# Optimization experiments

Hardware: AMD Instinct MI355X
Metric: run time of the kernel (lower is better)

Reference implementation:

```python
import jax, jax.numpy as jnp
import numpy as np

N, E = 50000, 800000
IN_DIM, HID, OUT_DIM, HEADS = 256, 128, 128, 2
EPS_BN = 1e-5


def _glorot(key, shape):
    fan_in, fan_out = shape[0], shape[-1]
    lim = float(np.sqrt(6.0 / (fan_in + fan_out)))
    return jax.random.uniform(key, shape, jnp.float32, -lim, lim)


def setup_inputs() -> dict:
    key = jax.random.key(0)
    ks = jax.random.split(key, 12)
    x = jax.random.normal(ks[0], (N, IN_DIM), jnp.float32)
    edge_index = jax.random.randint(ks[1], (2, E), 0, N, jnp.int64)
    return {
        "x": x,
        "edge_index": edge_index,
        # layer 1 (heads=2, concat)
        "W1": _glorot(ks[2], (IN_DIM, HEADS * HID)),
        "att_src1": _glorot(ks[3], (HEADS, HID)),
        "att_dst1": _glorot(ks[4], (HEADS, HID)),
        "b1": jnp.zeros((HEADS * HID,), jnp.float32),
        "g1": jnp.ones((HEADS * HID,), jnp.float32),
        "be1": jnp.zeros((HEADS * HID,), jnp.float32),
        # layer 2 (heads=1, no concat)
        "W2": _glorot(ks[5], (HEADS * HID, OUT_DIM)),
        "att_src2": _glorot(ks[6], (1, OUT_DIM)),
        "att_dst2": _glorot(ks[7], (1, OUT_DIM)),
        "b2": jnp.zeros((OUT_DIM,), jnp.float32),
        "g2": jnp.ones((OUT_DIM,), jnp.float32),
        "be2": jnp.zeros((OUT_DIM,), jnp.float32),
    }


def gat_conv(x, src, dst, W, att_src, att_dst, bias, heads, out_ch, concat):
    """PyG GATConv forward (dropout=identity at eval). Messages flow src->dst,
    softmax over incoming edges of dst, sum-aggregate."""
    h = (x @ W).reshape(-1, heads, out_ch)             # [N, H, C]
    a_s = jnp.einsum('nhc,hc->nh', h, att_src)          # [N, H]
    a_d = jnp.einsum('nhc,hc->nh', h, att_dst)
    e = jax.nn.leaky_relu(a_s[src] + a_d[dst], 0.2)     # [E, H]
    m = jax.ops.segment_max(e, dst, num_segments=N)     # [N, H]
    m = jnp.where(jnp.isfinite(m), m, 0.0)
    w = jnp.exp(e - m[dst])                             # [E, H]
    denom = jax.ops.segment_sum(w, dst, num_segments=N) # [N, H]
    alpha = w / (denom[dst] + 1e-16)                    # [E, H]
    msg = h[src] * alpha[:, :, None]                    # [E, H, C]
    out = jax.ops.segment_sum(msg, dst, num_segments=N) # [N, H, C]
    if concat:
        out = out.reshape(-1, heads * out_ch)
    else:
        out = out.mean(axis=1)
    return out + bias


def batchnorm_relu(x, gamma, beta):
    mu = x.mean(axis=0)
    var = x.var(axis=0)  # biased, as used for normalization in torch BN
    xn = (x - mu) * jax.lax.rsqrt(var + EPS_BN)
    return jax.nn.relu(xn * gamma + beta)


def reference(x, edge_index, W1, att_src1, att_dst1, b1, g1, be1,
              W2, att_src2, att_dst2, b2, g2, be2):
    src, dst = edge_index[0], edge_index[1]
    h = gat_conv(x, src, dst, W1, att_src1, att_dst1, b1, HEADS, HID, True)
    h = batchnorm_relu(h, g1, be1)
    h = gat_conv(h, src, dst, W2, att_src2, att_dst2, b2, 1, OUT_DIM, False)
    h = batchnorm_relu(h, g2, be2)
    return h
```

## Files before the change

kernel.cpp:

```cpp
#include <hip/hip_runtime.h>
#include <math.h>

#define IN_DIM 256
#define EPS_BN 1e-5f
#define NS 16

typedef __attribute__((ext_vector_type(8))) short short8v;
typedef __attribute__((ext_vector_type(4))) float f32x4;

__device__ __forceinline__ float lrelu(float v) { return v > 0.f ? v : 0.2f * v; }

__device__ __forceinline__ unsigned short f2bf(float f) {
    unsigned int u = __float_as_uint(f);
    u += 0x7fffu + ((u >> 16) & 1u);
    return (unsigned short)(u >> 16);
}
__device__ __forceinline__ float bf2f(unsigned short s) {
    return __uint_as_float((unsigned int)s << 16);
}

__device__ __forceinline__ void gld16(const void* g, void* l) {
    __builtin_amdgcn_global_load_lds((const __attribute__((address_space(1))) void*)g,
                                     (__attribute__((address_space(3))) void*)l, 16, 0, 0);
}

__device__ __forceinline__ int edge_at(const void* ei, int is64, long long i) {
    if (is64) return (int)((const long long*)ei)[i];
    return ((const int*)ei)[i];
}

__global__ __launch_bounds__(256) void prep_kernel(const float* __restrict__ x,
                                                   unsigned short* __restrict__ xb, long long n8,
                                                   const float* __restrict__ W1,
                                                   unsigned short* __restrict__ Wt1,
                                                   const float* __restrict__ W2,
                                                   unsigned short* __restrict__ Wt2,
                                                   const unsigned int* __restrict__ eiw,
                                                   int* __restrict__ flag, long long nwords) {
    __shared__ int nz;
    long long nbx = (n8 + 255) / 256;
    long long b = blockIdx.x;
    if (b < nbx) {
        long long i = b * 256 + threadIdx.x;
        if (i < n8) {
            const float4* p = (const float4*)(x + i * 8);
            float4 v0 = p[0], v1 = p[1];
            ushort4 o0, o1;
            o0.x = f2bf(v0.x); o0.y = f2bf(v0.y); o0.z = f2bf(v0.z); o0.w = f2bf(v0.w);
            o1.x = f2bf(v1.x); o1.y = f2bf(v1.y); o1.z = f2bf(v1.z); o1.w = f2bf(v1.w);
            *(ushort4*)(xb + i * 8) = o0;
            *(ushort4*)(xb + i * 8 + 4) = o1;
        }
        return;
    }
    b -= nbx;
    if (b < 256) {
        int idx = (int)b * 256 + threadIdx.x;
        int c = idx >> 8, k = idx & 255;
        Wt1[idx] = f2bf(W1[(long long)k * 256 + c]);
        return;
    }
    b -= 256;
    if (b < 128) {
        int idx = (int)b * 256 + threadIdx.x;
        int c = idx >> 8, k = idx & 255;
        Wt2[idx] = f2bf(W2[(long long)k * 128 + c]);
        return;
    }
    if (threadIdx.x == 0) nz = 0;
    __syncthreads();
    int cnt = 0;
    for (int i = 0; i < 4; i++) {
        long long idx = 2LL * (threadIdx.x + i * 256) + 1;
        if (idx < nwords && eiw[idx] != 0u) cnt++;
    }
    if (cnt) atomicAdd(&nz, 1);
    __syncthreads();
    if (threadIdx.x == 0) flag[0] = (nz == 0) ? 1 : 0;
}

__global__ void count_deg_kernel(const void* __restrict__ ei, const int* __restrict__ flag,
                                 int* __restrict__ deg, int E_) {
    int is64 = flag[0];
    int i = blockIdx.x * 256 + threadIdx.x;
    if (i < E_) {
        int d = edge_at(ei, is64, (long long)E_ + i);
        atomicAdd(&deg[d], 1);
    }
}

__global__ __launch_bounds__(256) void scan_partial_kernel(const int* __restrict__ deg,
                                                           int* __restrict__ bsum, int n) {
    __shared__ int sh[256];
    int t = threadIdx.x;
    int i = blockIdx.x * 256 + t;
    sh[t] = (i < n) ? deg[i] : 0;
    __syncthreads();
    for (int off = 128; off >= 1; off >>= 1) {
        if (t < off) sh[t] += sh[t + off];
        __syncthreads();
    }
    if (t == 0) bsum[blockIdx.x] = sh[0];
}

__global__ __launch_bounds__(256) void scan_write_kernel(const int* __restrict__ deg,
                                                         const int* __restrict__ bsum,
                                                         int* __restrict__ rowptr,
                                                         int* __restrict__ ctr, int n, int nb) {
    __shared__ int sh[256];
    __shared__ int base_sh;
    int t = threadIdx.x;
    int b = blockIdx.x;
    sh[t] = (t < b) ? bsum[t] : 0;
    __syncthreads();
    for (int off = 128; off >= 1; off >>= 1) {
        if (t < off) sh[t] += sh[t + off];
        __syncthreads();
    }
    if (t == 0) base_sh = sh[0];
    __syncthreads();
    int i = b * 256 + t;
    int d = (i < n) ? deg[i] : 0;
    sh[t] = d;
    __syncthreads();
    for (int off = 1; off < 256; off <<= 1) {
        int u = (t >= off) ? sh[t - off] : 0;
        __syncthreads();
        sh[t] += u;
        __syncthreads();
    }
    if (i < n) {
        int v = base_sh + sh[t] - d;
        rowptr[i] = v;
        ctr[i] = v;
    }
    if (b == nb - 1 && t == 255) rowptr[n] = base_sh + sh[255];
}

__global__ void scatter_kernel(const void* __restrict__ ei, const int* __restrict__ flag,
                               int* __restrict__ ctr, int* __restrict__ srcs, int E_) {
    int is64 = flag[0];
    int i = blockIdx.x * 256 + threadIdx.x;
    if (i < E_) {
        int s = edge_at(ei, is64, i);
        int d = edge_at(ei, is64, (long long)E_ + i);
        int pos = atomicAdd(&ctr[d], 1);
        srcs[pos] = s;
    }
}

template <int NCOL, int NH, bool FUSEBN>
__global__ __launch_bounds__(256) void gemm_mfma_kernel(const unsigned short* __restrict__ Ab,
                                                        const unsigned short* __restrict__ Wt,
                                                        unsigned short* __restrict__ C,
                                                        const float* __restrict__ att_s,
                                                        const float* __restrict__ att_d,
                                                        float* __restrict__ a_s,
                                                        float* __restrict__ a_d, int M,
                                                        const float* __restrict__ bnsh,
                                                        const float* __restrict__ gamma,
                                                        const float* __restrict__ beta) {
    __shared__ unsigned short B_lds[64 * 256];
    __shared__ unsigned short A_lds[128 * 64];
    __shared__ float scs[FUSEBN ? 256 : 1];
    __shared__ float shs[FUSEBN ? 256 : 1];
    const int t = threadIdx.x;
    const int w = t >> 6, l = t & 63;
    const int row0 = blockIdx.x * 128;
    const int col0 = blockIdx.y * 64;

    {
        const char* wb = (const char*)Wt + (size_t)col0 * 512;
#pragma unroll
        for (int it = 0; it < 8; ++it) {
            int q = w * 8 + it;
            int i = q * 64 + l;
            int r = i >> 5;
            int cs = (i & 31) ^ (r & 7);
            gld16(wb + (size_t)r * 512 + cs * 16, (char*)B_lds + q * 1024);
        }
    }

    short8v nxt[4];
    const char* ab = (const char*)Ab + (size_t)row0 * 512;

    if (FUSEBN) {
        {
            int c = t;
            float s = 0.f, q = 0.f;
#pragma unroll
            for (int sh = 0; sh < NS; sh++) { s += bnsh[sh * 512 + c]; q += bnsh[sh * 512 + 256 + c]; }
            float invN = 1.f / (float)M;
            float mu = s * invN;
            float var = q * invN - mu * mu;
            float sc = rsqrtf(var + EPS_BN) * gamma[c];
            scs[c] = sc;
            shs[c] = beta[c] - mu * sc;
        }
#pragma unroll
        for (int it = 0; it < 4; ++it) {
            int i = it * 256 + t;
            int r = i >> 3, g = i & 7;
            int gr = row0 + r;
            nxt[it] = (gr < M) ? *(const short8v*)(Ab + (size_t)gr * 256 + g * 8)
                               : (short8v)(short)0;
        }
        __syncthreads();
#pragma unroll
        for (int it = 0; it < 4; ++it) {
            int i = it * 256 + t;
            int r = i >> 3, g = i & 7;
            int kb = g * 8;
            float4 s0 = *(const float4*)&scs[kb], s1 = *(const float4*)&scs[kb + 4];
            float4 h0 = *(const float4*)&shs[kb], h1 = *(const float4*)&shs[kb + 4];
            short8v v = nxt[it];
            short8v ov;
            ov[0] = (short)f2bf(fmaxf(bf2f((unsigned short)v[0]) * s0.x + h0.x, 0.f));
            ov[1] = (short)f2bf(fmaxf(bf2f((unsigned short)v[1]) * s0.y + h0.y, 0.f));
            ov[2] = (short)f2bf(fmaxf(bf2f((unsigned short)v[2]) * s0.z + h0.z, 0.f));
            ov[3] = (short)f2bf(fmaxf(bf2f((unsigned short)v[3]) * s0.w + h0.w, 0.f));
            ov[4] = (short)f2bf(fmaxf(bf2f((unsigned short)v[4]) * s1.x + h1.x, 0.f));
            ov[5] = (short)f2bf(fmaxf(bf2f((unsigned short)v[5]) * s1.y + h1.y, 0.f));
            ov[6] = (short)f2bf(fmaxf(bf2f((unsigned short)v[6]) * s1.z + h1.z, 0.f));
            ov[7] = (short)f2bf(fmaxf(bf2f((unsigned short)v[7]) * s1.w + h1.w, 0.f));
            *(short8v*)((char*)A_lds + r * 128 + ((g ^ (r & 7)) << 4)) = ov;
        }
    } else {
#pragma unroll
        for (int it = 0; it < 4; ++it) {
            int q = w * 4 + it;
            int i = q * 64 + l;
            int r = i >> 3;
            int cs = (i & 7) ^ (r & 7);
            gld16(ab + (size_t)r * 512 + cs * 16, (char*)A_lds + q * 1024);
        }
    }
    __syncthreads();

    const int rl = l & 15, kg = l >> 4;
    f32x4 acc0[4], acc1[4];
#pragma unroll
    for (int i = 0; i < 4; ++i) { acc0[i] = (f32x4)(0.f); acc1[i] = (f32x4)(0.f); }

    const int ar0 = w * 32 + rl, ar1 = ar0 + 16;
    const int aswz = (ar0 & 7) << 4;

    for (int c = 0; c < 4; ++c) {
        if (FUSEBN && c < 3) {
#pragma unroll
            for (int it = 0; it < 4; ++it) {
                int i = it * 256 + t;
                int r = i >> 3, g = i & 7;
                int gr = row0 + r;
                nxt[it] = (gr < M) ? *(const short8v*)(Ab + (size_t)gr * 256 + (c + 1) * 64 + g * 8)
                                   : (short8v)(short)0;
            }
        }
#pragma unroll
        for (int s = 0; s < 2; ++s) {
            short8v a0 = *(const short8v*)((const char*)A_lds +
                          ((ar0 * 128 + s * 64 + kg * 16) ^ aswz));
            short8v a1 = *(const short8v*)((const char*)A_lds +
                          ((ar1 * 128 + s * 64 + kg * 16) ^ aswz));
#pragma unroll
            for (int ct = 0; ct < 4; ++ct) {
                int br = ct * 16 + rl;
                short8v bfr = *(const short8v*)((const char*)B_lds +
                               ((br * 512 + c * 128 + s * 64 + kg * 16) ^ ((br & 7) << 4)));
                acc0[ct] = __builtin_amdgcn_mfma_f32_16x16x32_bf16(a0, bfr, acc0[ct], 0, 0, 0);
                acc1[ct] = __builtin_amdgcn_mfma_f32_16x16x32_bf16(a1, bfr, acc1[ct], 0, 0, 0);
            }
        }
        __syncthreads();
        if (c < 3) {
            if (FUSEBN) {
#pragma unroll
                for (int it = 0; it < 4; ++it) {
                    int i = it * 256 + t;
                    int r = i >> 3, g = i & 7;
                    int kb = (c + 1) * 64 + g * 8;
                    float4 s0 = *(const float4*)&scs[kb], s1 = *(const float4*)&scs[kb + 4];
                    float4 h0 = *(const float4*)&shs[kb], h1 = *(const float4*)&shs[kb + 4];
                    short8v v = nxt[it];
                    short8v ov;
                    ov[0] = (short)f2bf(fmaxf(bf2f((unsigned short)v[0]) * s0.x + h0.x, 0.f));
                    ov[1] = (short)f2bf(fmaxf(bf2f((unsigned short)v[1]) * s0.y + h0.y, 0.f));
                    ov[2] = (short)f2bf(fmaxf(bf2f((unsigned short)v[2]) * s0.z + h0.z, 0.f));
                    ov[3] = (short)f2bf(fmaxf(bf2f((unsigned short)v[3]) * s0.w + h0.w, 0.f));
                    ov[4] = (short)f2bf(fmaxf(bf2f((unsigned short)v[4]) * s1.x + h1.x, 0.f));
                    ov[5] = (short)f2bf(fmaxf(bf2f((unsigned short)v[5]) * s1.y + h1.y, 0.f));
                    ov[6] = (short)f2bf(fmaxf(bf2f((unsigned short)v[6]) * s1.z + h1.z, 0.f));
                    ov[7] = (short)f2bf(fmaxf(bf2f((unsigned short)v[7]) * s1.w + h1.w, 0.f));
                    *(short8v*)((char*)A_lds + r * 128 + ((g ^ (r & 7)) << 4)) = ov;
                }
            } else {
#pragma unroll
                for (int it = 0; it < 4; ++it) {
                    int q = w * 4 + it;
                    int i = q * 64 + l;
                    int r = i >> 3;
                    int cs = (i & 7) ^ (r & 7);
                    gld16(ab + (size_t)r * 512 + (c + 1) * 128 + cs * 16, (char*)A_lds + q * 1024);
                }
            }
            __syncthreads();
        }
    }

#pragma unroll
    for (int ct = 0; ct < 4; ++ct) {
#pragma unroll
        for (int r = 0; r < 4; ++r) {
            int gr0 = row0 + w * 32 + kg * 4 + r;
            if (gr0 < M) C[(long long)gr0 * NCOL + col0 + ct * 16 + rl] = f2bf(acc0[ct][r]);
            int gr1 = gr0 + 16;
            if (gr1 < M) C[(long long)gr1 * NCOL + col0 + ct * 16 + rl] = f2bf(acc1[ct][r]);
        }
    }

    float asp0[4] = {}, adp0[4] = {}, asp1[4] = {}, adp1[4] = {};
#pragma unroll
    for (int ct = 0; ct < 4; ++ct) {
        int col = col0 + ct * 16 + rl;
        float vs = att_s[col], vd = att_d[col];
#pragma unroll
        for (int r = 0; r < 4; ++r) {
            asp0[r] += acc0[ct][r] * vs; adp0[r] += acc0[ct][r] * vd;
            asp1[r] += acc1[ct][r] * vs; adp1[r] += acc1[ct][r] * vd;
        }
    }
#pragma unroll
    for (int off = 1; off < 16; off <<= 1) {
#pragma unroll
        for (int r = 0; r < 4; ++r) {
            asp0[r] += __shfl_xor(asp0[r], off);
            adp0[r] += __shfl_xor(adp0[r], off);
            asp1[r] += __shfl_xor(asp1[r], off);
            adp1[r] += __shfl_xor(adp1[r], off);
        }
    }
    if (rl == 0) {
        int head = (NH == 2) ? (col0 >> 7) : 0;
#pragma unroll
        for (int r = 0; r < 4; ++r) {
            int gr0 = row0 + w * 32 + kg * 4 + r;
            if (gr0 < M) {
                atomicAdd(&a_s[gr0 * NH + head], asp0[r]);
                atomicAdd(&a_d[gr0 * NH + head], adp0[r]);
            }
            int gr1 = gr0 + 16;
            if (gr1 < M) {
                atomicAdd(&a_s[gr1 * NH + head], asp1[r]);
                atomicAdd(&a_d[gr1 * NH + head], adp1[r]);
            }
        }
    }
}

__global__ __launch_bounds__(256) void aggregate1_kernel(const unsigned short* __restrict__ h,
                                                         const int* __restrict__ rowptr,
                                                         const int* __restrict__ srcs,
                                                         const float* __restrict__ a_s,
                                                         const float* __restrict__ a_d,
                                                         const float* __restrict__ bias,
                                                         unsigned short* __restrict__ out,
                                                         float* __restrict__ bnsh, int Nn) {
    __shared__ float sw_lds[4][256];
    const int t = threadIdx.x;
    const int wid = t >> 6, lane = t & 63;
    const int hh = (lane >> 4) & 1;
    const int eb = lane >> 5;
    const int colb = (lane & 31) * 8;
    float* wbase = sw_lds[wid];
    float bnsum[8] = {}, bnsq[8] = {};
    const int stride = gridDim.x * 4;

    for (int n = blockIdx.x * 4 + wid; n < Nn; n += stride) {
        int beg = rowptr[n], end = rowptr[n + 1];
        float2 adv = *(const float2*)&a_d[(size_t)n * 2];
        float ad0 = adv.x, ad1 = adv.y;
        float acc[8] = {0.f, 0.f, 0.f, 0.f, 0.f, 0.f, 0.f, 0.f};
        float den = 0.f, m0 = -1e30f, m1 = -1e30f;

        for (int cb = beg; cb < end; cb += 64) {
            int cnt = end - cb; if (cnt > 64) cnt = 64;
            float e0 = -1e30f, e1 = -1e30f;
            int s_l = 0;
            if (lane < cnt) {
                s_l = srcs[cb + lane];
                float2 av = *(const float2*)&a_s[(size_t)s_l * 2];
                e0 = lrelu(av.x + ad0);
                e1 = lrelu(av.y + ad1);
            }
            float cm0 = e0, cm1 = e1;
            for (int off = 32; off >= 1; off >>= 1) {
                cm0 = fmaxf(cm0, __shfl_xor(cm0, off));
                cm1 = fmaxf(cm1, __shfl_xor(cm1, off));
            }
            if (cm0 > m0 || cm1 > m1) {
                float f0 = (cm0 > m0) ? __expf(m0 - cm0) : 1.f;
                float f1 = (cm1 > m1) ? __expf(m1 - cm1) : 1.f;
                m0 = fmaxf(m0, cm0); m1 = fmaxf(m1, cm1);
                float fo = hh ? f1 : f0;
#pragma unroll
                for (int j = 0; j < 8; j++) acc[j] *= fo;
                den *= fo;
            }
            if (lane < cnt) {
                *(float2*)&wbase[lane * 2] = make_float2(__int_as_float(s_l), __expf(e0 - m0));
                *(float2*)&wbase[128 + lane * 2] = make_float2(__int_as_float(s_l), __expf(e1 - m1));
            }
            int c = 0;
            for (; c + 8 <= cnt; c += 8) {
                float2 sw0 = *(const float2*)&wbase[hh * 128 + (c + eb) * 2];
                float2 sw1 = *(const float2*)&wbase[hh * 128 + (c + 2 + eb) * 2];
                float2 sw2 = *(const float2*)&wbase[hh * 128 + (c + 4 + eb) * 2];
                float2 sw3 = *(const float2*)&wbase[hh * 128 + (c + 6 + eb) * 2];
                short8v p0 = *(const short8v*)(h + ((size_t)__float_as_int(sw0.x) << 8) + colb);
                short8v p1 = *(const short8v*)(h + ((size_t)__float_as_int(sw1.x) << 8) + colb);
                short8v p2 = *(const short8v*)(h + ((size_t)__float_as_int(sw2.x) << 8) + colb);
                short8v p3 = *(const short8v*)(h + ((size_t)__float_as_int(sw3.x) << 8) + colb);
                den += sw0.y + sw1.y + sw2.y + sw3.y;
#pragma unroll
                for (int j = 0; j < 8; j++)
                    acc[j] += sw0.y * bf2f((unsigned short)p0[j]) + sw1.y * bf2f((unsigned short)p1[j])
                            + sw2.y * bf2f((unsigned short)p2[j]) + sw3.y * bf2f((unsigned short)p3[j]);
            }
            for (; c + 4 <= cnt; c += 4) {
                float2 sw0 = *(const float2*)&wbase[hh * 128 + (c + eb) * 2];
                float2 sw1 = *(const float2*)&wbase[hh * 128 + (c + 2 + eb) * 2];
                short8v p0 = *(const short8v*)(h + ((size_t)__float_as_int(sw0.x) << 8) + colb);
                short8v p1 = *(const short8v*)(h + ((size_t)__float_as_int(sw1.x) << 8) + colb);
                den += sw0.y + sw1.y;
#pragma unroll
                for (int j = 0; j < 8; j++)
                    acc[j] += sw0.y * bf2f((unsigned short)p0[j]) + sw1.y * bf2f((unsigned short)p1[j]);
            }
            for (; c < cnt; c += 2) {
                int e = c + eb;
                if (e < cnt) {
                    float2 sw0 = *(const float2*)&wbase[hh * 128 + e * 2];
                    short8v p0 = *(const short8v*)(h + ((size_t)__float_as_int(sw0.x) << 8) + colb);
                    den += sw0.y;
#pragma unroll
                    for (int j = 0; j < 8; j++) acc[j] += sw0.y * bf2f((unsigned short)p0[j]);
                }
            }
        }
        den += __shfl_xor(den, 32);
#pragma unroll
        for (int j = 0; j < 8; j++) acc[j] += __shfl_xor(acc[j], 32);
        if (lane < 32) {
            float inv = 1.f / (den + 1e-16f);
            float4 b0 = *(const float4*)&bias[colb];
            float4 b1 = *(const float4*)&bias[colb + 4];
            float of[8];
            of[0] = acc[0] * inv + b0.x; of[1] = acc[1] * inv + b0.y;
            of[2] = acc[2] * inv + b0.z; of[3] = acc[3] * inv + b0.w;
            of[4] = acc[4] * inv + b1.x; of[5] = acc[5] * inv + b1.y;
            of[6] = acc[6] * inv + b1.z; of[7] = acc[7] * inv + b1.w;
            short8v o;
#pragma unroll
            for (int j = 0; j < 8; j++) {
                o[j] = (short)f2bf(of[j]);
                bnsum[j] += of[j];
                bnsq[j] += of[j] * of[j];
            }
            *(short8v*)(out + ((size_t)n << 8) + colb) = o;
        }
    }

    __syncthreads();
    if (lane < 32) {
#pragma unroll
        for (int j = 0; j < 8; j++) wbase[colb + j] = bnsum[j];
    }
    __syncthreads();
    {
        int sh = (blockIdx.x & (NS - 1)) * 512;
        float s = sw_lds[0][t] + sw_lds[1][t] + sw_lds[2][t] + sw_lds[3][t];
        atomicAdd(&bnsh[sh + t], s);
    }
    __syncthreads();
    if (lane < 32) {
#pragma unroll
        for (int j = 0; j < 8; j++) wbase[colb + j] = bnsq[j];
    }
    __syncthreads();
    {
        int sh = (blockIdx.x & (NS - 1)) * 512;
        float q = sw_lds[0][t] + sw_lds[1][t] + sw_lds[2][t] + sw_lds[3][t];
        atomicAdd(&bnsh[sh + 256 + t], q);
    }
}

__global__ __launch_bounds__(256) void aggregate2_kernel(const unsigned short* __restrict__ h,
                                                         const int* __restrict__ rowptr,
                                                         const int* __restrict__ srcs,
                                                         const float* __restrict__ a_s,
                                                         const float* __restrict__ a_d,
                                                         const float* __restrict__ bias,
                                                         float* __restrict__ out,
                                                         float* __restrict__ bnsh, int Nn) {
    __shared__ float sw_lds[4][128];
    const int t = threadIdx.x;
    const int wid = t >> 6, lane = t & 63;
    const int eo = lane >> 4;
    const int colb = (lane & 15) * 8;
    float* wbase = sw_lds[wid];
    float bnsum[8] = {}, bnsq[8] = {};
    const int stride = gridDim.x * 4;

    for (int n = blockIdx.x * 4 + wid; n < Nn; n += stride) {
        int beg = rowptr[n], end = rowptr[n + 1];
        float ad = a_d[n];
        float acc[8] = {0.f, 0.f, 0.f, 0.f, 0.f, 0.f, 0.f, 0.f};
        float den = 0.f, m = -1e30f;

        for (int cb = beg; cb < end; cb += 64) {
            int cnt = end - cb; if (cnt > 64) cnt = 64;
            float e_ = -1e30f;
            int s_l = 0;
            if (lane < cnt) {
                s_l = srcs[cb + lane];
                e_ = lrelu(a_s[s_l] + ad);
            }
            float cm = e_;
            for (int off = 32; off >= 1; off >>= 1) cm = fmaxf(cm, __shfl_xor(cm, off));
            if (cm > m) {
                float f = __expf(m - cm);
                m = cm;
#pragma unroll
                for (int j = 0; j < 8; j++) acc[j] *= f;
                den *= f;
            }
            if (lane < cnt)
                *(float2*)&wbase[lane * 2] = make_float2(__int_as_float(s_l), __expf(e_ - m));
            int c = 0;
            for (; c + 16 <= cnt; c += 16) {
                float2 sw0 = *(const float2*)&wbase[(c + eo) * 2];
                float2 sw1 = *(const float2*)&wbase[(c + 4 + eo) * 2];
                float2 sw2 = *(const float2*)&wbase[(c + 8 + eo) * 2];
                float2 sw3 = *(const float2*)&wbase[(c + 12 + eo) * 2];
                short8v p0 = *(const short8v*)(h + ((size_t)__float_as_int(sw0.x) << 7) + colb);
                short8v p1 = *(const short8v*)(h + ((size_t)__float_as_int(sw1.x) << 7) + colb);
                short8v p2 = *(const short8v*)(h + ((size_t)__float_as_int(sw2.x) << 7) + colb);
                short8v p3 = *(const short8v*)(h + ((size_t)__float_as_int(sw3.x) << 7) + colb);
                den += sw0.y + sw1.y + sw2.y + sw3.y;
#pragma unroll
                for (int j = 0; j < 8; j++)
                    acc[j] += sw0.y * bf2f((unsigned short)p0[j]) + sw1.y * bf2f((unsigned short)p1[j])
                            + sw2.y * bf2f((unsigned short)p2[j]) + sw3.y * bf2f((unsigned short)p3[j]);
            }
            for (; c + 8 <= cnt; c += 8) {
                float2 sw0 = *(const float2*)&wbase[(c + eo) * 2];
                float2 sw1 = *(const float2*)&wbase[(c + 4 + eo) * 2];
                short8v p0 = *(const short8v*)(h + ((size_t)__float_as_int(sw0.x) << 7) + colb);
                short8v p1 = *(const short8v*)(h + ((size_t)__float_as_int(sw1.x) << 7) + colb);
                den += sw0.y + sw1.y;
#pragma unroll
                for (int j = 0; j < 8; j++)
                    acc[j] += sw0.y * bf2f((unsigned short)p0[j]) + sw1.y * bf2f((unsigned short)p1[j]);
            }
            for (; c < cnt; c += 4) {
                int e = c + eo;
                if (e < cnt) {
                    float2 sw0 = *(const float2*)&wbase[e * 2];
                    short8v p0 = *(const short8v*)(h + ((size_t)__float_as_int(sw0.x) << 7) + colb);
                    den += sw0.y;
#pragma unroll
                    for (int j = 0; j < 8; j++) acc[j] += sw0.y * bf2f((unsigned short)p0[j]);
                }
            }
        }
        den += __shfl_xor(den, 16);
        den += __shfl_xor(den, 32);
#pragma unroll
        for (int j = 0; j < 8; j++) {
            acc[j] += __shfl_xor(acc[j], 16);
            acc[j] += __shfl_xor(acc[j], 32);
        }
        if (lane < 16) {
            float inv = 1.f / (den + 1e-16f);
            float4 b0 = *(const float4*)&bias[colb];
            float4 b1 = *(const float4*)&bias[colb + 4];
            float of[8];
            of[0] = acc[0] * inv + b0.x; of[1] = acc[1] * inv + b0.y;
            of[2] = acc[2] * inv + b0.z; of[3] = acc[3] * inv + b0.w;
            of[4] = acc[4] * inv + b1.x; of[5] = acc[5] * inv + b1.y;
            of[6] = acc[6] * inv + b1.z; of[7] = acc[7] * inv + b1.w;
#pragma unroll
            for (int j = 0; j < 8; j++) {
                bnsum[j] += of[j];
                bnsq[j] += of[j] * of[j];
            }
            float* ob = out + (size_t)n * 128 + colb;
            *(float4*)ob = make_float4(of[0], of[1], of[2], of[3]);
            *(float4*)(ob + 4) = make_float4(of[4], of[5], of[6], of[7]);
        }
    }

    __syncthreads();
    if (lane < 16) {
#pragma unroll
        for (int j = 0; j < 8; j++) wbase[colb + j] = bnsum[j];
    }
    __syncthreads();
    if (t < 128) {
        int sh = (blockIdx.x & (NS - 1)) * 256;
        float s = sw_lds[0][t] + sw_lds[1][t] + sw_lds[2][t] + sw_lds[3][t];
        atomicAdd(&bnsh[sh + t], s);
    }
    __syncthreads();
    if (lane < 16) {
#pragma unroll
        for (int j = 0; j < 8; j++) wbase[colb + j] = bnsq[j];
    }
    __syncthreads();
    if (t < 128) {
        int sh = (blockIdx.x & (NS - 1)) * 256;
        float q = sw_lds[0][t] + sw_lds[1][t] + sw_lds[2][t] + sw_lds[3][t];
        atomicAdd(&bnsh[sh + 128 + t], q);
    }
}

__global__ __launch_bounds__(256) void bn_apply_final_kernel(float* __restrict__ x,
                                                             const float* __restrict__ bnsh,
                                                             const float* __restrict__ gamma,
                                                             const float* __restrict__ beta,
                                                             int Nn) {
    int t = threadIdx.x;
    int col = t & 127;
    float s = 0.f, q = 0.f;
#pragma unroll
    for (int sh = 0; sh < NS; sh++) { s += bnsh[sh * 256 + col]; q += bnsh[sh * 256 + 128 + col]; }
    float mu = s / (float)Nn;
    float var = q / (float)Nn - mu * mu;
    float sc = rsqrtf(var + EPS_BN) * gamma[col];
    float sh_ = beta[col] - mu * sc;
    int r0 = blockIdx.x * 2 + (t >> 7);
    int rs = gridDim.x * 2;
    for (int r = r0; r < Nn; r += rs) {
        size_t idx = (size_t)r * 128 + col;
        x[idx] = fmaxf(x[idx] * sc + sh_, 0.f);
    }
}

extern "C" void kernel_launch(void* const* d_in, const int* in_sizes, int n_in,
                              void* d_out, int out_size, void* d_ws, size_t ws_size,
                              hipStream_t stream) {
    const float* x        = (const float*)d_in[0];
    const void*  ei       = d_in[1];
    const float* W1       = (const float*)d_in[2];
    const float* att_src1 = (const float*)d_in[3];
    const float* att_dst1 = (const float*)d_in[4];
    const float* b1       = (const float*)d_in[5];
    const float* g1       = (const float*)d_in[6];
    const float* be1      = (const float*)d_in[7];
    const float* W2       = (const float*)d_in[8];
    const float* att_src2 = (const float*)d_in[9];
    const float* att_dst2 = (const float*)d_in[10];
    const float* b2       = (const float*)d_in[11];
    const float* g2       = (const float*)d_in[12];
    const float* be2      = (const float*)d_in[13];

    const int Nn = in_sizes[0] / IN_DIM;
    const int E_ = in_sizes[1] / 2;
    const int gb = (Nn + 127) / 128;
    const int Mpad = gb * 128 + 128;

    char* ws = (char*)d_ws;
    size_t o = 0;
    auto alloc = [&](size_t bytes) {
        size_t r = o;
        o += (bytes + 255) & ~(size_t)255;
        return r;
    };
    int* flag = (int*)(ws + alloc(4));
    size_t z0 = o;
    int*   deg   = (int*)(ws + alloc((size_t)Nn * 4));
    float* as1   = (float*)(ws + alloc((size_t)Nn * 2 * 4));
    float* ad1   = (float*)(ws + alloc((size_t)Nn * 2 * 4));
    float* as2   = (float*)(ws + alloc((size_t)Nn * 4));
    float* ad2   = (float*)(ws + alloc((size_t)Nn * 4));
    float* bn1sh = (float*)(ws + alloc((size_t)NS * 512 * 4));
    float* bn2sh = (float*)(ws + alloc((size_t)NS * 256 * 4));
    size_t z1 = o;
    int*   rowptr = (int*)(ws + alloc((size_t)(Nn + 1) * 4));
    int*   ctr    = (int*)(ws + alloc((size_t)Nn * 4));
    int*   srcs   = (int*)(ws + alloc((size_t)E_ * 4));
    int*   bsum   = (int*)(ws + alloc(256 * 4));
    unsigned short* Wt1  = (unsigned short*)(ws + alloc((size_t)256 * 256 * 2));
    unsigned short* Wt2  = (unsigned short*)(ws + alloc((size_t)128 * 256 * 2));
    unsigned short* xb   = (unsigned short*)(ws + alloc((size_t)Mpad * 256 * 2));
    unsigned short* x2b0 = (unsigned short*)(ws + alloc((size_t)Nn * 256 * 2));
    unsigned short* h1b  = (unsigned short*)(ws + alloc((size_t)Nn * 256 * 2));
    unsigned short* h2b  = (unsigned short*)(ws + alloc((size_t)Nn * 128 * 2));
    float* outf = (float*)d_out;

    hipMemsetAsync(ws + z0, 0, z1 - z0, stream);

    {
        long long n8 = (long long)Nn * 256 / 8;
        long long grid = (n8 + 255) / 256 + 256 + 128 + 1;
        prep_kernel<<<(int)grid, 256, 0, stream>>>(x, xb, n8, W1, Wt1, W2, Wt2,
                                                   (const unsigned int*)ei, flag,
                                                   (long long)2 * E_);
    }

    int eb = (E_ + 255) / 256;
    int nsb = (Nn + 255) / 256;
    count_deg_kernel<<<eb, 256, 0, stream>>>(ei, flag, deg, E_);
    scan_partial_kernel<<<nsb, 256, 0, stream>>>(deg, bsum, Nn);
    scan_write_kernel<<<nsb, 256, 0, stream>>>(deg, bsum, rowptr, ctr, Nn, nsb);
    scatter_kernel<<<eb, 256, 0, stream>>>(ei, flag, ctr, srcs, E_);

    const int agg_blocks = 2048;

    gemm_mfma_kernel<256, 2, false><<<dim3(gb, 4), 256, 0, stream>>>(
        xb, Wt1, h1b, att_src1, att_dst1, as1, ad1, Nn, nullptr, nullptr, nullptr);
    aggregate1_kernel<<<agg_blocks, 256, 0, stream>>>(h1b, rowptr, srcs, as1, ad1, b1, x2b0,
                                                      bn1sh, Nn);

    gemm_mfma_kernel<128, 1, true><<<dim3(gb, 2), 256, 0, stream>>>(
        x2b0, Wt2, h2b, att_src2, att_dst2, as2, ad2, Nn, bn1sh, g1, be1);
    aggregate2_kernel<<<agg_blocks, 256, 0, stream>>>(h2b, rowptr, srcs, as2, ad2, b2, outf,
                                                      bn2sh, Nn);
    bn_apply_final_kernel<<<512, 256, 0, stream>>>(outf, bn2sh, g2, be2, Nn);
}
```

Before: 295.6 us.

## Merge CSR build and final BN into cooperative grid-synced kernels

Replaces the memset, prep, degree count, two-pass scan and scatter launches with one cooperative kernel that separates the phases with grid.sync, and folds the final batchnorm apply into the layer-2 aggregation kernel after a grid-wide sync. It also rewrites the bf16 accumulation in both aggregation kernels to unpack packed 32-bit words with shifts and masks into float2 FMAs. The aim is to cut kernel launch gaps and unpacking overhead, at the cost of persistent grids sized from occupancy, which may lower parallelism in the edge-heavy phases, plus the cost of each grid barrier.

Measured after the change: 924.9 us. 213% more time.

```diff
diff --git a/kernel.cpp b/kernel.cpp
--- a/kernel.cpp
+++ b/kernel.cpp
@@ -1,5 +1,8 @@
 #include <hip/hip_runtime.h>
+#include <hip/hip_cooperative_groups.h>
 #include <math.h>
+
+namespace cg = cooperative_groups;
 
 #define IN_DIM 256
 #define EPS_BN 1e-5f
@@ -19,6 +22,11 @@
     return __uint_as_float((unsigned int)s << 16);
 }
 
+__device__ __forceinline__ void bfma(float2& a, unsigned int pw, float w) {
+    a.x = fmaf(__uint_as_float(pw << 16), w, a.x);
+    a.y = fmaf(__uint_as_float(pw & 0xffff0000u), w, a.y);
+}
+
 __device__ __forceinline__ void gld16(const void* g, void* l) {
     __builtin_amdgcn_global_load_lds((const __attribute__((address_space(1))) void*)g,
                                      (__attribute__((address_space(3))) void*)l, 16, 0, 0);
@@ -29,119 +37,109 @@
     return ((const int*)ei)[i];
 }
 
-__global__ __launch_bounds__(256) void prep_kernel(const float* __restrict__ x,
-                                                   unsigned short* __restrict__ xb, long long n8,
-                                                   const float* __restrict__ W1,
-                                                   unsigned short* __restrict__ Wt1,
-                                                   const float* __restrict__ W2,
-                                                   unsigned short* __restrict__ Wt2,
-                                                   const unsigned int* __restrict__ eiw,
-                                                   int* __restrict__ flag, long long nwords) {
+__global__ __launch_bounds__(256) void build_kernel(
+    const float* __restrict__ x, unsigned short* __restrict__ xb, long long n8,
+    const float* __restrict__ W1, unsigned short* __restrict__ Wt1,
+    const float* __restrict__ W2, unsigned short* __restrict__ Wt2,
+    const void* __restrict__ ei, int* __restrict__ flag,
+    float* __restrict__ zbase, long long zcnt4,
+    int* __restrict__ deg, int* __restrict__ bsum,
+    int* __restrict__ rowptr, int* __restrict__ ctr, int* __restrict__ srcs,
+    int Nn, int E_, int nsb) {
+    __shared__ int sh[256];
+    __shared__ int base_sh;
     __shared__ int nz;
-    long long nbx = (n8 + 255) / 256;
-    long long b = blockIdx.x;
-    if (b < nbx) {
-        long long i = b * 256 + threadIdx.x;
-        if (i < n8) {
-            const float4* p = (const float4*)(x + i * 8);
-            float4 v0 = p[0], v1 = p[1];
-            ushort4 o0, o1;
-            o0.x = f2bf(v0.x); o0.y = f2bf(v0.y); o0.z = f2bf(v0.z); o0.w = f2bf(v0.w);
-            o1.x = f2bf(v1.x); o1.y = f2bf(v1.y); o1.z = f2bf(v1.z); o1.w = f2bf(v1.w);
-            *(ushort4*)(xb + i * 8) = o0;
-            *(ushort4*)(xb + i * 8 + 4) = o1;
-        }
-        return;
-    }
-    b -= nbx;
-    if (b < 256) {
-        int idx = (int)b * 256 + threadIdx.x;
-        int c = idx >> 8, k = idx & 255;
-        Wt1[idx] = f2bf(W1[(long long)k * 256 + c]);
-        return;
-    }
-    b -= 256;
-    if (b < 128) {
-        int idx = (int)b * 256 + threadIdx.x;
-        int c = idx >> 8, k = idx & 255;
-        Wt2[idx] = f2bf(W2[(long long)k * 128 + c]);
-        return;
-    }
-    if (threadIdx.x == 0) nz = 0;
-    __syncthreads();
-    int cnt = 0;
-    for (int i = 0; i < 4; i++) {
-        long long idx = 2LL * (threadIdx.x + i * 256) + 1;
-        if (idx < nwords && eiw[idx] != 0u) cnt++;
-    }
-    if (cnt) atomicAdd(&nz, 1);
-    __syncthreads();
-    if (threadIdx.x == 0) flag[0] = (nz == 0) ? 1 : 0;
-}
-
-__global__ void count_deg_kernel(const void* __restrict__ ei, const int* __restrict__ flag,
-                                 int* __restrict__ deg, int E_) {
-    int is64 = flag[0];
-    int i = blockIdx.x * 256 + threadIdx.x;
-    if (i < E_) {
+    const int t = threadIdx.x;
+    const int nb = gridDim.x;
+    const long long tstride = (long long)nb * 256;
+    cg::grid_group grid = cg::this_grid();
+
+    for (long long i = (long long)blockIdx.x * 256 + t; i < zcnt4; i += tstride)
+        *(float4*)(zbase + i * 4) = make_float4(0.f, 0.f, 0.f, 0.f);
+    const long long nbx = (n8 + 255) / 256;
+    const long long totA = nbx + 256 + 128 + 1;
+    for (long long vb = blockIdx.x; vb < totA; vb += nb) {
+        if (vb < nbx) {
+            long long i = vb * 256 + t;
+            if (i < n8) {
+                const float4* p = (const float4*)(x + i * 8);
+                float4 v0 = p[0], v1 = p[1];
+                ushort4 o0, o1;
+                o0.x = f2bf(v0.x); o0.y = f2bf(v0.y); o0.z = f2bf(v0.z); o0.w = f2bf(v0.w);
+                o1.x = f2bf(v1.x); o1.y = f2bf(v1.y); o1.z = f2bf(v1.z); o1.w = f2bf(v1.w);
+                *(ushort4*)(xb + i * 8) = o0;
+                *(ushort4*)(xb + i * 8 + 4) = o1;
+            }
+        } else if (vb < nbx + 256) {
+            int idx = (int)(vb - nbx) * 256 + t;
+            int c = idx >> 8, k = idx & 255;
+            Wt1[idx] = f2bf(W1[(long long)k * 256 + c]);
+        } else if (vb < nbx + 384) {
+            int idx = (int)(vb - nbx - 256) * 256 + t;
+            int c = idx >> 8, k = idx & 255;
+            Wt2[idx] = f2bf(W2[(long long)k * 128 + c]);
+        } else {
+            if (t == 0) nz = 0;
+            __syncthreads();
+            const unsigned int* w = (const unsigned int*)ei;
+            int cnt = 0;
+            for (int i2 = 0; i2 < 4; i2++) {
+                long long idx = 2LL * (t + i2 * 256) + 1;
+                if (idx < 2LL * E_ && w[idx] != 0u) cnt++;
+            }
+            if (cnt) atomicAdd(&nz, 1);
+            __syncthreads();
+            if (t == 0) flag[0] = (nz == 0) ? 1 : 0;
+        }
+    }
+    grid.sync();
+    const int is64 = flag[0];
+    for (long long i = (long long)blockIdx.x * 256 + t; i < E_; i += tstride) {
         int d = edge_at(ei, is64, (long long)E_ + i);
         atomicAdd(&deg[d], 1);
     }
-}
-
-__global__ __launch_bounds__(256) void scan_partial_kernel(const int* __restrict__ deg,
-                                                           int* __restrict__ bsum, int n) {
-    __shared__ int sh[256];
-    int t = threadIdx.x;
-    int i = blockIdx.x * 256 + t;
-    sh[t] = (i < n) ? deg[i] : 0;
-    __syncthreads();
-    for (int off = 128; off >= 1; off >>= 1) {
-        if (t < off) sh[t] += sh[t + off];
+    grid.sync();
+    for (int vb = blockIdx.x; vb < nsb; vb += nb) {
         __syncthreads();
-    }
-    if (t == 0) bsum[blockIdx.x] = sh[0];
-}
-
-__global__ __launch_bounds__(256) void scan_write_kernel(const int* __restrict__ deg,
-                                                         const int* __restrict__ bsum,
-                                                         int* __restrict__ rowptr,
-                                                         int* __restrict__ ctr, int n, int nb) {
-    __shared__ int sh[256];
-    __shared__ int base_sh;
-    int t = threadIdx.x;
-    int b = blockIdx.x;
-    sh[t] = (t < b) ? bsum[t] : 0;
-    __syncthreads();
-    for (int off = 128; off >= 1; off >>= 1) {
-        if (t < off) sh[t] += sh[t + off];
+        int i = vb * 256 + t;
+        sh[t] = (i < Nn) ? deg[i] : 0;
         __syncthreads();
-    }
-    if (t == 0) base_sh = sh[0];
-    __syncthreads();
-    int i = b * 256 + t;
-    int d = (i < n) ? deg[i] : 0;
-    sh[t] = d;
-    __syncthreads();
-    for (int off = 1; off < 256; off <<= 1) {
-        int u = (t >= off) ? sh[t - off] : 0;
+        for (int off = 128; off >= 1; off >>= 1) {
+            if (t < off) sh[t] += sh[t + off];
+            __syncthreads();
+        }
+        if (t == 0) bsum[vb] = sh[0];
+    }
+    grid.sync();
+    for (int vb = blockIdx.x; vb < nsb; vb += nb) {
         __syncthreads();
-        sh[t] += u;
+        sh[t] = (t < vb) ? bsum[t] : 0;
         __syncthreads();
-    }
-    if (i < n) {
-        int v = base_sh + sh[t] - d;
-        rowptr[i] = v;
-        ctr[i] = v;
-    }
-    if (b == nb - 1 && t == 255) rowptr[n] = base_sh + sh[255];
-}
-
-__global__ void scatter_kernel(const void* __restrict__ ei, const int* __restrict__ flag,
-                               int* __restrict__ ctr, int* __restrict__ srcs, int E_) {
-    int is64 = flag[0];
-    int i = blockIdx.x * 256 + threadIdx.x;
-    if (i < E_) {
+        for (int off = 128; off >= 1; off >>= 1) {
+            if (t < off) sh[t] += sh[t + off];
+            __syncthreads();
+        }
+        if (t == 0) base_sh = sh[0];
+        __syncthreads();
+        int i = vb * 256 + t;
+        int d = (i < Nn) ? deg[i] : 0;
+        sh[t] = d;
+        __syncthreads();
+        for (int off = 1; off < 256; off <<= 1) {
+            int u = (t >= off) ? sh[t - off] : 0;
+            __syncthreads();
+            sh[t] += u;
+            __syncthreads();
+        }
+        if (i < Nn) {
+            int v = base_sh + sh[t] - d;
+            rowptr[i] = v;
+            ctr[i] = v;
+        }
+        if (vb == nsb - 1 && t == 255) rowptr[Nn] = base_sh + sh[255];
+    }
+    grid.sync();
+    for (long long i = (long long)blockIdx.x * 256 + t; i < E_; i += tstride) {
         int s = edge_at(ei, is64, i);
         int d = edge_at(ei, is64, (long long)E_ + i);
         int pos = atomicAdd(&ctr[d], 1);
@@ -372,14 +370,14 @@
     const int eb = lane >> 5;
     const int colb = (lane & 31) * 8;
     float* wbase = sw_lds[wid];
-    float bnsum[8] = {}, bnsq[8] = {};
+    float2 bnsum2[4] = {}, bnsq2[4] = {};
     const int stride = gridDim.x * 4;
 
     for (int n = blockIdx.x * 4 + wid; n < Nn; n += stride) {
         int beg = rowptr[n], end = rowptr[n + 1];
         float2 adv = *(const float2*)&a_d[(size_t)n * 2];
         float ad0 = adv.x, ad1 = adv.y;
-        float acc[8] = {0.f, 0.f, 0.f, 0.f, 0.f, 0.f, 0.f, 0.f};
+        float2 acc2[4] = {};
         float den = 0.f, m0 = -1e30f, m1 = -1e30f;
 
         for (int cb = beg; cb < end; cb += 64) {
@@ -403,7 +401,7 @@
                 m0 = fmaxf(m0, cm0); m1 = fmaxf(m1, cm1);
                 float fo = hh ? f1 : f0;
 #pragma unroll
-                for (int j = 0; j < 8; j++) acc[j] *= fo;
+                for (int j = 0; j < 4; j++) { acc2[j].x *= fo; acc2[j].y *= fo; }
                 den *= fo;
             }
             if (lane < cnt) {
@@ -416,55 +414,65 @@
                 float2 sw1 = *(const float2*)&wbase[hh * 128 + (c + 2 + eb) * 2];
                 float2 sw2 = *(const float2*)&wbase[hh * 128 + (c + 4 + eb) * 2];
                 float2 sw3 = *(const float2*)&wbase[hh * 128 + (c + 6 + eb) * 2];
-                short8v p0 = *(const short8v*)(h + ((size_t)__float_as_int(sw0.x) << 8) + colb);
-                short8v p1 = *(const short8v*)(h + ((size_t)__float_as_int(sw1.x) << 8) + colb);
-                short8v p2 = *(const short8v*)(h + ((size_t)__float_as_int(sw2.x) << 8) + colb);
-                short8v p3 = *(const short8v*)(h + ((size_t)__float_as_int(sw3.x) << 8) + colb);
+                uint4 p0 = *(const uint4*)(h + ((size_t)__float_as_int(sw0.x) << 8) + colb);
+                uint4 p1 = *(const uint4*)(h + ((size_t)__float_as_int(sw1.x) << 8) + colb);
+                uint4 p2 = *(const uint4*)(h + ((size_t)__float_as_int(sw2.x) << 8) + colb);
+                uint4 p3 = *(const uint4*)(h + ((size_t)__float_as_int(sw3.x) << 8) + colb);
                 den += sw0.y + sw1.y + sw2.y + sw3.y;
-#pragma unroll
-                for (int j = 0; j < 8; j++)
-                    acc[j] += sw0.y * bf2f((unsigned short)p0[j]) + sw1.y * bf2f((unsigned short)p1[j])
-                            + sw2.y * bf2f((unsigned short)p2[j]) + sw3.y * bf2f((unsigned short)p3[j]);
+                bfma(acc2[0], p0.x, sw0.y); bfma(acc2[1], p0.y, sw0.y);
+                bfma(acc2[2], p0.z, sw0.y); bfma(acc2[3], p0.w, sw0.y);
+                bfma(acc2[0], p1.x, sw1.y); bfma(acc2[1], p1.y, sw1.y);
+                bfma(acc2[2], p1.z, sw1.y); bfma(acc2[3], p1.w, sw1.y);
+                bfma(acc2[0], p2.x, sw2.y); bfma(acc2[1], p2.y, sw2.y);
+                bfma(acc2[2], p2.z, sw2.y); bfma(acc2[3], p2.w, sw2.y);
+                bfma(acc2[0], p3.x, sw3.y); bfma(acc2[1], p3.y, sw3.y);
+                bfma(acc2[2], p3.z, sw3.y); bfma(acc2[3], p3.w, sw3.y);
             }
             for (; c + 4 <= cnt; c += 4) {
                 float2 sw0 = *(const float2*)&wbase[hh * 128 + (c + eb) * 2];
                 float2 sw1 = *(const float2*)&wbase[hh * 128 + (c + 2 + eb) * 2];
-                short8v p0 = *(const short8v*)(h + ((size_t)__float_as_int(sw0.x) << 8) + colb);
-                short8v p1 = *(const short8v*)(h + ((size_t)__float_as_int(sw1.x) << 8) + colb);
+                uint4 p0 = *(const uint4*)(h + ((size_t)__float_as_int(sw0.x) << 8) + colb);
+                uint4 p1 = *(const uint4*)(h + ((size_t)__float_as_int(sw1.x) << 8) + colb);
                 den += sw0.y + sw1.y;
-#pragma unroll
-                for (int j = 0; j < 8; j++)
-                    acc[j] += sw0.y * bf2f((unsigned short)p0[j]) + sw1.y * bf2f((unsigned short)p1[j]);
+                bfma(acc2[0], p0.x, sw0.y); bfma(acc2[1], p0.y, sw0.y);
+                bfma(acc2[2], p0.z, sw0.y); bfma(acc2[3], p0.w, sw0.y);
+                bfma(acc2[0], p1.x, sw1.y); bfma(acc2[1], p1.y, sw1.y);
+                bfma(acc2[2], p1.z, sw1.y); bfma(acc2[3], p1.w, sw1.y);
             }
             for (; c < cnt; c += 2) {
                 int e = c + eb;
                 if (e < cnt) {
                     float2 sw0 = *(const float2*)&wbase[hh * 128 + e * 2];
-                    short8v p0 = *(const short8v*)(h + ((size_t)__float_as_int(sw0.x) << 8) + colb);
+                    uint4 p0 = *(const uint4*)(h + ((size_t)__float_as_int(sw0.x) << 8) + colb);
                     den += sw0.y;
-#pragma unroll
-                    for (int j = 0; j < 8; j++) acc[j] += sw0.y * bf2f((unsigned short)p0[j]);
+                    bfma(acc2[0], p0.x, sw0.y); bfma(acc2[1], p0.y, sw0.y);
+                    bfma(acc2[2], p0.z, sw0.y); bfma(acc2[3], p0.w, sw0.y);
                 }
             }
         }
         den += __shfl_xor(den, 32);
 #pragma unroll
-        for (int j = 0; j < 8; j++) acc[j] += __shfl_xor(acc[j], 32);
+        for (int j = 0; j < 4; j++) {
+            acc2[j].x += __shfl_xor(acc2[j].x, 32);
+            acc2[j].y += __shfl_xor(acc2[j].y, 32);
+        }
         if (lane < 32) {
             float inv = 1.f / (den + 1e-16f);
             float4 b0 = *(const float4*)&bias[colb];
             float4 b1 = *(const float4*)&bias[colb + 4];
             float of[8];
-            of[0] = acc[0] * inv + b0.x; of[1] = acc[1] * inv + b0.y;
-            of[2] = acc[2] * inv + b0.z; of[3] = acc[3] * inv + b0.w;
-            of[4] = acc[4] * inv + b1.x; of[5] = acc[5] * inv + b1.y;
-            of[6] = acc[6] * inv + b1.z; of[7] = acc[7] * inv + b1.w;
+            of[0] = acc2[0].x * inv + b0.x; of[1] = acc2[0].y * inv + b0.y;
+            of[2] = acc2[1].x * inv + b0.z; of[3] = acc2[1].y * inv + b0.w;
+            of[4] = acc2[2].x * inv + b1.x; of[5] = acc2[2].y * inv + b1.y;
+            of[6] = acc2[3].x * inv + b1.z; of[7] = acc2[3].y * inv + b1.w;
             short8v o;
 #pragma unroll
-            for (int j = 0; j < 8; j++) {
-                o[j] = (short)f2bf(of[j]);
-                bnsum[j] += of[j];
-                bnsq[j] += of[j] * of[j];
+            for (int j = 0; j < 4; j++) {
+                o[2 * j] = (short)f2bf(of[2 * j]);
+                o[2 * j + 1] = (short)f2bf(of[2 * j + 1]);
+                bnsum2[j].x += of[2 * j];     bnsum2[j].y += of[2 * j + 1];
+                bnsq2[j].x += of[2 * j] * of[2 * j];
+                bnsq2[j].y += of[2 * j + 1] * of[2 * j + 1];
             }
             *(short8v*)(out + ((size_t)n << 8) + colb) = o;
         }
@@ -473,7 +481,10 @@
     __syncthreads();
     if (lane < 32) {
 #pragma unroll
-        for (int j = 0; j < 8; j++) wbase[colb + j] = bnsum[j];
+        for (int j = 0; j < 4; j++) {
+            wbase[colb + 2 * j] = bnsum2[j].x;
+            wbase[colb + 2 * j + 1] = bnsum2[j].y;
+        }
     }
     __syncthreads();
     {
@@ -484,7 +495,10 @@
     __syncthreads();
     if (lane < 32) {
 #pragma unroll
-        for (int j = 0; j < 8; j++) wbase[colb + j] = bnsq[j];
+        for (int j = 0; j < 4; j++) {
+            wbase[colb + 2 * j] = bnsq2[j].x;
+            wbase[colb + 2 * j + 1] = bnsq2[j].y;
+        }
     }
     __syncthreads();
     {
@@ -494,27 +508,29 @@
     }
 }
 
-__global__ __launch_bounds__(256) void aggregate2_kernel(const unsigned short* __restrict__ h,
-                                                         const int* __restrict__ rowptr,
-                                                         const int* __restrict__ srcs,
-                                                         const float* __restrict__ a_s,
-                                                         const float* __restrict__ a_d,
-                                                         const float* __restrict__ bias,
-                                                         float* __restrict__ out,
-                                                         float* __restrict__ bnsh, int Nn) {
+__global__ __launch_bounds__(256) void agg2bn_kernel(const unsigned short* __restrict__ h,
+                                                     const int* __restrict__ rowptr,
+                                                     const int* __restrict__ srcs,
+                                                     const float* __restrict__ a_s,
+                                                     const float* __restrict__ a_d,
+                                                     const float* __restrict__ bias,
+                                                     float* __restrict__ out,
+                                                     float* __restrict__ bnsh,
+                                                     const float* __restrict__ gamma,
+                                                     const float* __restrict__ beta, int Nn) {
     __shared__ float sw_lds[4][128];
     const int t = threadIdx.x;
     const int wid = t >> 6, lane = t & 63;
     const int eo = lane >> 4;
     const int colb = (lane & 15) * 8;
     float* wbase = sw_lds[wid];
-    float bnsum[8] = {}, bnsq[8] = {};
+    float2 bnsum2[4] = {}, bnsq2[4] = {};
     const int stride = gridDim.x * 4;
 
     for (int n = blockIdx.x * 4 + wid; n < Nn; n += stride) {
         int beg = rowptr[n], end = rowptr[n + 1];
         float ad = a_d[n];
-        float acc[8] = {0.f, 0.f, 0.f, 0.f, 0.f, 0.f, 0.f, 0.f};
+        float2 acc2[4] = {};
         float den = 0.f, m = -1e30f;
 
         for (int cb = beg; cb < end; cb += 64) {
@@ -531,7 +547,7 @@
                 float f = __expf(m - cm);
                 m = cm;
 #pragma unroll
-                for (int j = 0; j < 8; j++) acc[j] *= f;
+                for (int j = 0; j < 4; j++) { acc2[j].x *= f; acc2[j].y *= f; }
                 den *= f;
             }
             if (lane < cnt)
@@ -542,57 +558,65 @@
                 float2 sw1 = *(const float2*)&wbase[(c + 4 + eo) * 2];
                 float2 sw2 = *(const float2*)&wbase[(c + 8 + eo) * 2];
                 float2 sw3 = *(const float2*)&wbase[(c + 12 + eo) * 2];
-                short8v p0 = *(const short8v*)(h + ((size_t)__float_as_int(sw0.x) << 7) + colb);
-                short8v p1 = *(const short8v*)(h + ((size_t)__float_as_int(sw1.x) << 7) + colb);
-                short8v p2 = *(const short8v*)(h + ((size_t)__float_as_int(sw2.x) << 7) + colb);
-                short8v p3 = *(const short8v*)(h + ((size_t)__float_as_int(sw3.x) << 7) + colb);
+                uint4 p0 = *(const uint4*)(h + ((size_t)__float_as_int(sw0.x) << 7) + colb);
+                uint4 p1 = *(const uint4*)(h + ((size_t)__float_as_int(sw1.x) << 7) + colb);
+                uint4 p2 = *(const uint4*)(h + ((size_t)__float_as_int(sw2.x) << 7) + colb);
+                uint4 p3 = *(const uint4*)(h + ((size_t)__float_as_int(sw3.x) << 7) + colb);
                 den += sw0.y + sw1.y + sw2.y + sw3.y;
-#pragma unroll
-                for (int j = 0; j < 8; j++)
-                    acc[j] += sw0.y * bf2f((unsigned short)p0[j]) + sw1.y * bf2f((unsigned short)p1[j])
-                            + sw2.y * bf2f((unsigned short)p2[j]) + sw3.y * bf2f((unsigned short)p3[j]);
+                bfma(acc2[0], p0.x, sw0.y); bfma(acc2[1], p0.y, sw0.y);
+                bfma(acc2[2], p0.z, sw0.y); bfma(acc2[3], p0.w, sw0.y);
+                bfma(acc2[0], p1.x, sw1.y); bfma(acc2[1], p1.y, sw1.y);
+                bfma(acc2[2], p1.z, sw1.y); bfma(acc2[3], p1.w, sw1.y);
+                bfma(acc2[0], p2.x, sw2.y); bfma(acc2[1], p2.y, sw2.y);
+                bfma(acc2[2], p2.z, sw2.y); bfma(acc2[3], p2.w, sw2.y);
+                bfma(acc2[0], p3.x, sw3.y); bfma(acc2[1], p3.y, sw3.y);
+                bfma(acc2[2], p3.z, sw3.y); bfma(acc2[3], p3.w, sw3.y);
             }
             for (; c + 8 <= cnt; c += 8) {
                 float2 sw0 = *(const float2*)&wbase[(c + eo) * 2];
                 float2 sw1 = *(const float2*)&wbase[(c + 4 + eo) * 2];
-                short8v p0 = *(const short8v*)(h + ((size_t)__float_as_int(sw0.x) << 7) + colb);
-                short8v p1 = *(const short8v*)(h + ((size_t)__float_as_int(sw1.x) << 7) + colb);
+                uint4 p0 = *(const uint4*)(h + ((size_t)__float_as_int(sw0.x) << 7) + colb);
+                uint4 p1 = *(const uint4*)(h + ((size_t)__float_as_int(sw1.x) << 7) + colb);
                 den += sw0.y + sw1.y;
-#pragma unroll
-                for (int j = 0; j < 8; j++)
-                    acc[j] += sw0.y * bf2f((unsigned short)p0[j]) + sw1.y * bf2f((unsigned short)p1[j]);
+                bfma(acc2[0], p0.x, sw0.y); bfma(acc2[1], p0.y, sw0.y);
+                bfma(acc2[2], p0.z, sw0.y); bfma(acc2[3], p0.w, sw0.y);
+                bfma(acc2[0], p1.x, sw1.y); bfma(acc2[1], p1.y, sw1.y);
+                bfma(acc2[2], p1.z, sw1.y); bfma(acc2[3], p1.w, sw1.y);
             }
             for (; c < cnt; c += 4) {
                 int e = c + eo;
                 if (e < cnt) {
                     float2 sw0 = *(const float2*)&wbase[e * 2];
-                    short8v p0 = *(const short8v*)(h + ((size_t)__float_as_int(sw0.x) << 7) + colb);
+                    uint4 p0 = *(const uint4*)(h + ((size_t)__float_as_int(sw0.x) << 7) + colb);
                     den += sw0.y;
-#pragma unroll
-                    for (int j = 0; j < 8; j++) acc[j] += sw0.y * bf2f((unsigned short)p0[j]);
+                    bfma(acc2[0], p0.x, sw0.y); bfma(acc2[1], p0.y, sw0.y);
+                    bfma(acc2[2], p0.z, sw0.y); bfma(acc2[3], p0.w, sw0.y);
                 }
             }
         }
         den += __shfl_xor(den, 16);
         den += __shfl_xor(den, 32);
 #pragma unroll
-        for (int j = 0; j < 8; j++) {
-            acc[j] += __shfl_xor(acc[j], 16);
-            acc[j] += __shfl_xor(acc[j], 32);
+        for (int j = 0; j < 4; j++) {
+            acc2[j].x += __shfl_xor(acc2[j].x, 16);
+            acc2[j].x += __shfl_xor(acc2[j].x, 32);
+            acc2[j].y += __shfl_xor(acc2[j].y, 16);
+            acc2[j].y += __shfl_xor(acc2[j].y, 32);
         }
         if (lane < 16) {
             float inv = 1.f / (den + 1e-16f);
             float4 b0 = *(const float4*)&bias[colb];
             float4 b1 = *(const float4*)&bias[colb + 4];
             float of[8];
-            of[0] = acc[0] * inv + b0.x; of[1] = acc[1] * inv + b0.y;
-            of[2] = acc[2] * inv + b0.z; of[3] = acc[3] * inv + b0.w;
-            of[4] = acc[4] * inv + b1.x; of[5] = acc[5] * inv + b1.y;
-            of[6] = acc[6] * inv + b1.z; of[7] = acc[7] * inv + b1.w;
-#pragma unroll
-            for (int j = 0; j < 8; j++) {
-                bnsum[j] += of[j];
-                bnsq[j] += of[j] * of[j];
+            of[0] = acc2[0].x * inv + b0.x; of[1] = acc2[0].y * inv + b0.y;
+            of[2] = acc2[1].x * inv + b0.z; of[3] = acc2[1].y * inv + b0.w;
+            of[4] = acc2[2].x * inv + b1.x; of[5] = acc2[2].y * inv + b1.y;
+            of[6] = acc2[3].x * inv + b1.z; of[7] = acc2[3].y * inv + b1.w;
+#pragma unroll
+            for (int j = 0; j < 4; j++) {
+                bnsum2[j].x += of[2 * j];     bnsum2[j].y += of[2 * j + 1];
+                bnsq2[j].x += of[2 * j] * of[2 * j];
+                bnsq2[j].y += of[2 * j + 1] * of[2 * j + 1];
             }
             float* ob = out + (size_t)n * 128 + colb;
             *(float4*)ob = make_float4(of[0], of[1], of[2], of[3]);
@@ -603,7 +627,10 @@
     __syncthreads();
     if (lane < 16) {
 #pragma unroll
-        for (int j = 0; j < 8; j++) wbase[colb + j] = bnsum[j];
+        for (int j = 0; j < 4; j++) {
+            wbase[colb + 2 * j] = bnsum2[j].x;
+            wbase[colb + 2 * j + 1] = bnsum2[j].y;
+        }
     }
     __syncthreads();
     if (t < 128) {
@@ -614,7 +641,10 @@
     __syncthreads();
     if (lane < 16) {
 #pragma unroll
-        for (int j = 0; j < 8; j++) wbase[colb + j] = bnsq[j];
+        for (int j = 0; j < 4; j++) {
+            wbase[colb + 2 * j] = bnsq2[j].x;
+            wbase[colb + 2 * j + 1] = bnsq2[j].y;
+        }
     }
     __syncthreads();
     if (t < 128) {
@@ -622,27 +652,26 @@
         float q = sw_lds[0][t] + sw_lds[1][t] + sw_lds[2][t] + sw_lds[3][t];
         atomicAdd(&bnsh[sh + 128 + t], q);
     }
-}
-
-__global__ __launch_bounds__(256) void bn_apply_final_kernel(float* __restrict__ x,
-                                                             const float* __restrict__ bnsh,
-                                                             const float* __restrict__ gamma,
-                                                             const float* __restrict__ beta,
-                                                             int Nn) {
-    int t = threadIdx.x;
-    int col = t & 127;
-    float s = 0.f, q = 0.f;
-#pragma unroll
-    for (int sh = 0; sh < NS; sh++) { s += bnsh[sh * 256 + col]; q += bnsh[sh * 256 + 128 + col]; }
-    float mu = s / (float)Nn;
-    float var = q / (float)Nn - mu * mu;
-    float sc = rsqrtf(var + EPS_BN) * gamma[col];
-    float sh_ = beta[col] - mu * sc;
-    int r0 = blockIdx.x * 2 + (t >> 7);
-    int rs = gridDim.x * 2;
-    for (int r = r0; r < Nn; r += rs) {
-        size_t idx = (size_t)r * 128 + col;
-        x[idx] = fmaxf(x[idx] * sc + sh_, 0.f);
+
+    cg::this_grid().sync();
+    {
+        int col = t & 127;
+        float s = 0.f, q = 0.f;
+#pragma unroll
+        for (int sh2 = 0; sh2 < NS; sh2++) {
+            s += bnsh[sh2 * 256 + col];
+            q += bnsh[sh2 * 256 + 128 + col];
+        }
+        float mu = s / (float)Nn;
+        float var = q / (float)Nn - mu * mu;
+        float sc = rsqrtf(var + EPS_BN) * gamma[col];
+        float sb = beta[col] - mu * sc;
+        int r0 = blockIdx.x * 2 + (t >> 7);
+        int rs = gridDim.x * 2;
+        for (int r = r0; r < Nn; r += rs) {
+            size_t idx = (size_t)r * 128 + col;
+            out[idx] = fmaxf(out[idx] * sc + sb, 0.f);
+        }
     }
 }
 
@@ -668,6 +697,7 @@
     const int E_ = in_sizes[1] / 2;
     const int gb = (Nn + 127) / 128;
     const int Mpad = gb * 128 + 128;
+    const int nsb = (Nn + 255) / 256;
 
     char* ws = (char*)d_ws;
     size_t o = 0;
@@ -697,34 +727,38 @@
     unsigned short* h1b  = (unsigned short*)(ws + alloc((size_t)Nn * 256 * 2));
     unsigned short* h2b  = (unsigned short*)(ws + alloc((size_t)Nn * 128 * 2));
     float* outf = (float*)d_out;
-
-    hipMemsetAsync(ws + z0, 0, z1 - z0, stream);
+    float* zbase = (float*)(ws + z0);
+    long long zcnt4 = (long long)(z1 - z0) / 16;
+    long long n8 = (long long)Nn * 256 / 8;
+
+    int nbB = 0, nbA = 0;
+    hipOccupancyMaxActiveBlocksPerMultiprocessor(&nbB, build_kernel, 256, 0);
+    hipOccupancyMaxActiveBlocksPerMultiprocessor(&nbA, agg2bn_kernel, 256, 0);
+    int gridB = (nbB > 0 ? nbB : 4) * 256; if (gridB > 2048) gridB = 2048;
+    int gridA = (nbA > 0 ? nbA : 4) * 256; if (gridA > 2048) gridA = 2048;
 
     {
-        long long n8 = (long long)Nn * 256 / 8;
-        long long grid = (n8 + 255) / 256 + 256 + 128 + 1;
-        prep_kernel<<<(int)grid, 256, 0, stream>>>(x, xb, n8, W1, Wt1, W2, Wt2,
-                                                   (const unsigned int*)ei, flag,
-                                                   (long long)2 * E_);
-    }
-
-    int eb = (E_ + 255) / 256;
-    int nsb = (Nn + 255) / 256;
-    count_deg_kernel<<<eb, 256, 0, stream>>>(ei, flag, deg, E_);
-    scan_partial_kernel<<<nsb, 256, 0, stream>>>(deg, bsum, Nn);
-    scan_write_kernel<<<nsb, 256, 0, stream>>>(deg, bsum, rowptr, ctr, Nn, nsb);
-    scatter_kernel<<<eb, 256, 0, stream>>>(ei, flag, ctr, srcs, E_);
-
-    const int agg_blocks = 2048;
+        void* argsB[] = {(void*)&x, (void*)&xb, (void*)&n8, (void*)&W1, (void*)&Wt1,
+                         (void*)&W2, (void*)&Wt2, (void*)&ei, (void*)&flag,
+                         (void*)&zbase, (void*)&zcnt4, (void*)&deg, (void*)&bsum,
+                         (void*)&rowptr, (void*)&ctr, (void*)&srcs,
+                         (void*)&Nn, (void*)&E_, (void*)&nsb};
+        hipLaunchCooperativeKernel((const void*)build_kernel, dim3(gridB), dim3(256),
+                                   argsB, 0, stream);
+    }
 
     gemm_mfma_kernel<256, 2, false><<<dim3(gb, 4), 256, 0, stream>>>(
         xb, Wt1, h1b, att_src1, att_dst1, as1, ad1, Nn, nullptr, nullptr, nullptr);
-    aggregate1_kernel<<<agg_blocks, 256, 0, stream>>>(h1b, rowptr, srcs, as1, ad1, b1, x2b0,
-                                                      bn1sh, Nn);
+    aggregate1_kernel<<<2048, 256, 0, stream>>>(h1b, rowptr, srcs, as1, ad1, b1, x2b0,
+                                                bn1sh, Nn);
 
     gemm_mfma_kernel<128, 1, true><<<dim3(gb, 2), 256, 0, stream>>>(
         x2b0, Wt2, h2b, att_src2, att_dst2, as2, ad2, Nn, bn1sh, g1, be1);
-    aggregate2_kernel<<<agg_blocks, 256, 0, stream>>>(h2b, rowptr, srcs, as2, ad2, b2, outf,
-                                                      bn2sh, Nn);
-    bn_apply_final_kernel<<<512, 256, 0, stream>>>(outf, bn2sh, g2, be2, Nn);
-}
+    {
+        void* argsA[] = {(void*)&h2b, (void*)&rowptr, (void*)&srcs, (void*)&as2,
+                         (void*)&ad2, (void*)&b2, (void*)&outf, (void*)&bn2sh,
+                         (void*)&g2, (void*)&be2, (void*)&Nn};
+        hipLaunchCooperativeKernel((const void*)agg2bn_kernel, dim3(gridA), dim3(256),
+                                   argsA, 0, stream);
+    }
+}
```
